# Performance work log

Hardware: AMD Instinct MI355X
Metric: run time of the kernel (lower is better)

## Reference

```python
import jax, jax.numpy as jnp
import numpy as np

D_MODEL = 512
HEAD_NUM = 8
EPS = 1e-5


def setup_inputs() -> dict:
    key = jax.random.key(0)
    ks = jax.random.split(key, 7)
    B, S, D = 2, 4096, D_MODEL
    scale = 1.0 / np.sqrt(D)
    return {
        "x": jax.random.normal(ks[0], (B, S, D), dtype=jnp.float32),
        "Wq": jax.random.normal(ks[1], (D, D), dtype=jnp.float32) * scale,
        "bq": jnp.zeros((D,), dtype=jnp.float32),
        "Wk": jax.random.normal(ks[2], (D, D), dtype=jnp.float32) * scale,
        "bk": jnp.zeros((D,), dtype=jnp.float32),
        "Wv": jax.random.normal(ks[3], (D, D), dtype=jnp.float32) * scale,
        "bv": jnp.zeros((D,), dtype=jnp.float32),
        "gamma": jnp.ones((D,), dtype=jnp.float32),
        "beta": jnp.zeros((D,), dtype=jnp.float32),
    }


def reference(x, Wq, bq, Wk, bk, Wv, bv, gamma, beta):
    B, S, D = x.shape
    H = HEAD_NUM
    hd = D // H  # q_k_head_dim == v_head_dim == 64
    q = (x @ Wq + bq).reshape(B, H, S, hd)  # faithful to torch .view (no transpose)
    k = (x @ Wk + bk).reshape(B, H, S, hd)
    v = (x @ Wv + bv).reshape(B, H, S, hd)
    # [B,H,S,S] score matrix, materialized exactly as the original does
    scores = jnp.einsum("bhqd,bhkd->bhqk", q, k) / jnp.sqrt(jnp.float32(hd))
    attn_w = jax.nn.softmax(scores, axis=-1)
    attn = jnp.einsum("bhqk,bhkd->bhqd", attn_w, v).reshape(B, S, D)
    h = x + attn
    mu = jnp.mean(h, axis=-1, keepdims=True)
    var = jnp.var(h, axis=-1, keepdims=True)
    y = (h - mu) / jnp.sqrt(var + EPS) * gamma + beta
    return y
```

## Files before the change

### kernel.cpp

```cpp
#include <hip/hip_runtime.h>
#include <stdint.h>

#define D_ 512
#define S_ 4096
#define HD 64
#define CHUNK (S_*HD)

typedef short short8 __attribute__((ext_vector_type(8)));
typedef unsigned short ushort8 __attribute__((ext_vector_type(8)));
typedef float f32x16 __attribute__((ext_vector_type(16)));
typedef float f32x4 __attribute__((ext_vector_type(4)));

__device__ __forceinline__ float b2f(unsigned short u){
  unsigned x = ((unsigned)u) << 16;
  return __builtin_bit_cast(float, x);
}
__device__ __forceinline__ unsigned short f2b(float f){
  unsigned x = __builtin_bit_cast(unsigned, f);
  return (unsigned short)((x + 0x7fffu + ((x >> 16) & 1u)) >> 16);
}
__device__ __forceinline__ unsigned cvt_pk_bf16(float lo, float hi){
  unsigned r; asm("v_cvt_pk_bf16_f32 %0, %1, %2" : "=v"(r) : "v"(lo), "v"(hi)); return r;
}
__device__ __forceinline__ float fexp2(float x){
  float r; asm("v_exp_f32 %0, %1" : "=v"(r) : "v"(x)); return r;
}
__device__ __forceinline__ void gload16(const void* g, void* l){
  __builtin_amdgcn_global_load_lds((__attribute__((address_space(1))) void*)g,
                                   (__attribute__((address_space(3))) void*)l, 16, 0, 0);
}

__global__ void k_convert(const float* __restrict__ x, unsigned short* __restrict__ xb,
                          const float* __restrict__ Wq, const float* __restrict__ Wk,
                          const float* __restrict__ Wv, unsigned short* __restrict__ wt){
  __shared__ __align__(16) float t[32][33];
  if (blockIdx.x < 2048){
    int i = blockIdx.x * blockDim.x + threadIdx.x;
    const float4* xv = (const float4*)x;
    float4 a = xv[i*2], b = xv[i*2+1];
    ushort8 o;
    o[0]=f2b(a.x); o[1]=f2b(a.y); o[2]=f2b(a.z); o[3]=f2b(a.w);
    o[4]=f2b(b.x); o[5]=f2b(b.y); o[6]=f2b(b.z); o[7]=f2b(b.w);
    ((ushort8*)xb)[i] = o;
    return;
  }
  const int i = blockIdx.x - 2048;
  const int z = i >> 8, rem = i & 255;
  const int k0 = (rem & 15) * 32, n0 = (rem >> 4) * 32;
  const float* W = (z==0) ? Wq : ((z==1) ? Wk : Wv);
  unsigned short* o = wt + z * D_ * D_;
  int r = threadIdx.x >> 3, c4 = (threadIdx.x & 7) * 4;
  float4 vv = *(const float4*)&W[(k0+r)*D_ + n0 + c4];
  t[r][c4+0]=vv.x; t[r][c4+1]=vv.y; t[r][c4+2]=vv.z; t[r][c4+3]=vv.w;
  __syncthreads();
  unsigned short* dst = &o[(n0+r)*D_ + k0 + c4];
  dst[0]=f2b(t[c4+0][r]); dst[1]=f2b(t[c4+1][r]);
  dst[2]=f2b(t[c4+2][r]); dst[3]=f2b(t[c4+3][r]);
}

__global__ void __launch_bounds__(256) k_gemm(const unsigned short* __restrict__ xb,
                                              const unsigned short* __restrict__ wt,
                                              const float* __restrict__ bq,
                                              const float* __restrict__ bk,
                                              const float* __restrict__ bv,
                                              unsigned short* __restrict__ q,
                                              unsigned short* __restrict__ k,
                                              unsigned short* __restrict__ v){
  __shared__ __align__(16) unsigned short At[2][128*32];
  __shared__ __align__(16) unsigned short Bt[2][128*32];
  const int bid = blockIdx.x;
  const int swz = (bid & 7) * 96 + (bid >> 3);
  const int mat = swz >> 8;
  const int rem = swz & 255;
  const int bx = rem >> 2, by = rem & 3;
  const unsigned short* w = wt + mat * D_ * D_;
  const float* bias = (mat==0) ? bq : ((mat==1) ? bk : bv);
  unsigned short* out = (mat==0) ? q : ((mat==1) ? k : v);
  const int m0 = bx * 128, n0 = by * 128;
  const int tid = threadIdx.x, lane = tid & 63, wv = tid >> 6;
  const int wm = wv >> 1, wn = wv & 1;
  const int l15 = lane & 15, l4 = lane >> 4;

  f32x4 acc[4][4] = {};

  auto stage = [&](int kt, int sel){
    const int kbase = kt * 32;
    #pragma unroll
    for (int j = 0; j < 2; j++){
      const int loff = wv*2048 + j*1024 + lane*16;
      const int row = loff >> 6;
      const int c = (loff >> 4) & 3;
      gload16(xb + (m0+row)*D_ + kbase + ((c ^ (row&3)) << 3),
              (char*)At[sel] + wv*2048 + j*1024);
      gload16(w  + (n0+row)*D_ + kbase + ((c ^ (row&3)) << 3),
              (char*)Bt[sel] + wv*2048 + j*1024);
    }
  };

  stage(0, 0);
  int buf = 0;
  for (int kt = 0; kt < 16; ++kt){
    __syncthreads();
    if (kt + 1 < 16) stage(kt + 1, buf ^ 1);
    short8 af[4], bf[4];
    #pragma unroll
    for (int mf = 0; mf < 4; mf++){
      const int row = wm*64 + mf*16 + l15;
      af[mf] = *(const short8*)((const char*)At[buf] + row*64 + ((l4*16) ^ ((row&3)<<4)));
    }
    #pragma unroll
    for (int nf = 0; nf < 4; nf++){
      const int row = wn*64 + nf*16 + l15;
      bf[nf] = *(const short8*)((const char*)Bt[buf] + row*64 + ((l4*16) ^ ((row&3)<<4)));
    }
    #pragma unroll
    for (int mf = 0; mf < 4; mf++)
      #pragma unroll
      for (int nf = 0; nf < 4; nf++)
        acc[mf][nf] = __builtin_amdgcn_mfma_f32_16x16x32_bf16(af[mf], bf[nf], acc[mf][nf], 0,0,0);
    buf ^= 1;
  }
  #pragma unroll
  for (int nf = 0; nf < 4; nf++){
    const int n = n0 + wn*64 + nf*16 + l15;
    const float bval = bias[n];
    #pragma unroll
    for (int mf = 0; mf < 4; mf++){
      #pragma unroll
      for (int r = 0; r < 4; r++){
        const int m = m0 + wm*64 + mf*16 + l4*4 + r;
        out[m*D_ + n] = f2b(acc[mf][nf][r] + bval);
      }
    }
  }
}

__global__ void k_transpose_v(const unsigned short* __restrict__ v, unsigned short* __restrict__ vt){
  __shared__ __align__(16) unsigned short t[64][72];
  const int bh = blockIdx.y, s0 = blockIdx.x * 64;
  const unsigned short* vc = v + bh * CHUNK;
  unsigned short* vtc = vt + bh * CHUNK;
  const int tid = threadIdx.x;
  #pragma unroll
  for (int j = 0; j < 2; j++){
    const int e = j*2048 + tid*8;
    const int row = e >> 6, col = e & 63;
    *(ushort8*)&t[row][col] = *(const ushort8*)&vc[(s0+row)*HD + col];
  }
  __syncthreads();
  const int d = tid >> 2, sc0 = (tid & 3) * 16;
  ushort8 o0, o1;
  #pragma unroll
  for (int j = 0; j < 4; j++){
    o0[j]   = t[sc0 + j     ][d];
    o0[j+4] = t[sc0 + 8 + j ][d];
    o1[j]   = t[sc0 + 4 + j ][d];
    o1[j+4] = t[sc0 + 12 + j][d];
  }
  *(ushort8*)&vtc[d*S_ + s0 + sc0]     = o0;
  *(ushort8*)&vtc[d*S_ + s0 + sc0 + 8] = o1;
}

__global__ void __launch_bounds__(256, 4) k_attn_part(const unsigned short* __restrict__ q,
                                                      const unsigned short* __restrict__ k,
                                                      const unsigned short* __restrict__ vt,
                                                      unsigned short* __restrict__ Op0,
                                                      unsigned short* __restrict__ Op1,
                                                      float2* __restrict__ ml0,
                                                      float2* __restrict__ ml1){
  __shared__ __align__(16) char smem[32768];
  const int bid = blockIdx.x;
  const int c8 = bid & 7, j = bid >> 3;
  const int bh   = 2*c8 + (j & 1);
  const int qblk = (j >> 1) & 31;
  const int half = (j >> 6) & 1;

  const int tid = threadIdx.x, lane = tid & 63, wv = tid >> 6;
  const int l31 = lane & 31, hi = lane >> 5;
  const unsigned short* qc  = q  + bh * CHUNK;
  const unsigned short* kc  = k  + bh * CHUNK;
  const unsigned short* vtc = vt + bh * CHUNK;
  unsigned short* Op = half ? Op1 : Op0;
  float2* ml = half ? ml1 : ml0;
  const int q0 = qblk * 128 + wv * 32;
  const int kvbase = half * 2048;

  short8 qf[4];
  {
    const int row = q0 + l31;
    #pragma unroll
    for (int kb = 0; kb < 4; kb++){
      ushort8 raw = *(const ushort8*)(qc + row*HD + kb*16 + hi*8);
      union { ushort8 u; short8 s; } cc;
      #pragma unroll
      for (int jj = 0; jj < 8; jj++) cc.u[jj] = f2b(b2f(raw[jj]) * (0.125f * 1.44269504f));
      qf[kb] = cc.s;
    }
  }
  short8 ones;
  #pragma unroll
  for (int jj = 0; jj < 8; jj++) ones[jj] = (short)0x3F80;

  f32x16 o0 = {}; f32x16 o1 = {};
  f32x16 lacc = {};
  float mrun = -__builtin_inff();

  auto stage = [&](int t, int sel){
    const int kv0 = kvbase + t * 64;
    char* kb_ = smem + sel*8192 + wv*2048;
    char* vb_ = smem + 16384 + sel*8192 + wv*2048;
    #pragma unroll
    for (int jj = 0; jj < 2; jj++){
      const int loff = wv*2048 + jj*1024 + lane*16;
      const int row = loff >> 7;
      const int c = (loff >> 4) & 7;
      gload16(kc  + (kv0+row)*HD + ((c ^ (row&7)) << 3), kb_ + jj*1024);
      gload16(vtc + row*S_ + kv0 + ((c ^ (row&7)) << 3), vb_ + jj*1024);
    }
  };

  stage(0, 0);
  int buf = 0;
  const int NT = 2048 / 64;
  for (int t = 0; t < NT; ++t){
    __syncthreads();
    if (t + 1 < NT) stage(t + 1, buf ^ 1);
    const char* kbuf = smem + buf*8192;
    const char* vbuf = smem + 16384 + buf*8192;

    f32x16 st0 = {}; f32x16 st1 = {};
    const int xr = (l31 & 7) << 4;
    #pragma unroll
    for (int kb = 0; kb < 4; kb++){
      const int off = kb*32 + hi*16;
      short8 kf0 = *(const short8*)(kbuf + l31*128        + (off ^ xr));
      short8 kf1 = *(const short8*)(kbuf + (32+l31)*128   + (off ^ xr));
      st0 = __builtin_amdgcn_mfma_f32_32x32x16_bf16(kf0, qf[kb], st0, 0,0,0);
      st1 = __builtin_amdgcn_mfma_f32_32x32x16_bf16(kf1, qf[kb], st1, 0,0,0);
    }

    float n0_ = fmaxf(fmaxf(st0[0], st0[1]),  st0[2]);
    float n1_ = fmaxf(fmaxf(st0[3], st0[4]),  st0[5]);
    float n2_ = fmaxf(fmaxf(st0[6], st0[7]),  st0[8]);
    float n3_ = fmaxf(fmaxf(st0[9], st0[10]), st0[11]);
    float n4_ = fmaxf(fmaxf(st0[12],st0[13]), st0[14]);
    float n5_ = fmaxf(fmaxf(st0[15],st1[0]),  st1[1]);
    float n6_ = fmaxf(fmaxf(st1[2], st1[3]),  st1[4]);
    float n7_ = fmaxf(fmaxf(st1[5], st1[6]),  st1[7]);
    float n8_ = fmaxf(fmaxf(st1[8], st1[9]),  st1[10]);
    float n9_ = fmaxf(fmaxf(st1[11],st1[12]), st1[13]);
    float nA_ = fmaxf(st1[14], st1[15]);
    n0_ = fmaxf(fmaxf(n0_, n1_), n2_);
    n3_ = fmaxf(fmaxf(n3_, n4_), n5_);
    n6_ = fmaxf(fmaxf(n6_, n7_), n8_);
    n9_ = fmaxf(n9_, nA_);
    float pm = fmaxf(fmaxf(fmaxf(n0_, n3_), n6_), n9_);
    pm = fmaxf(pm, __shfl_xor(pm, 32));

    if (!__all(pm <= mrun + 10.0f)){
      const float mn = fmaxf(mrun, pm);
      const float corr = fexp2(mrun - mn);
      mrun = mn;
      lacc[0] *= corr;
      o0 *= corr; o1 *= corr;
    }

    st0 -= mrun;
    st1 -= mrun;
    #pragma unroll
    for (int r = 0; r < 16; r++){
      st0[r] = fexp2(st0[r]);
      st1[r] = fexp2(st1[r]);
    }

    short8 pf[4];
    #pragma unroll
    for (int kb = 0; kb < 4; kb++){
      const f32x16& s = (kb < 2) ? st0 : st1;
      const int rb = (kb & 1) * 8;
      union { unsigned u[4]; short8 s8; } pu;
      pu.u[0] = cvt_pk_bf16(s[rb+0], s[rb+1]);
      pu.u[1] = cvt_pk_bf16(s[rb+2], s[rb+3]);
      pu.u[2] = cvt_pk_bf16(s[rb+4], s[rb+5]);
      pu.u[3] = cvt_pk_bf16(s[rb+6], s[rb+7]);
      pf[kb] = pu.s8;
    }

    #pragma unroll
    for (int kb = 0; kb < 4; kb++){
      const int off = kb*32 + hi*16;
      short8 vf0 = *(const short8*)(vbuf + l31*128      + (off ^ xr));
      short8 vf1 = *(const short8*)(vbuf + (32+l31)*128 + (off ^ xr));
      o0   = __builtin_amdgcn_mfma_f32_32x32x16_bf16(vf0, pf[kb], o0, 0,0,0);
      o1   = __builtin_amdgcn_mfma_f32_32x32x16_bf16(vf1, pf[kb], o1, 0,0,0);
      lacc = __builtin_amdgcn_mfma_f32_32x32x16_bf16(ones, pf[kb], lacc, 0,0,0);
    }
    buf ^= 1;
  }

  __syncthreads();
  {
    float* po = (float*)(void*)smem + wv*2048;
    #pragma unroll
    for (int r = 0; r < 16; r++){
      const int d = (r&3) + 8*(r>>2) + 4*hi;
      po[l31*64 + d]      = o0[r];
      po[l31*64 + 32 + d] = o1[r];
    }
  }
  if (hi == 0){
    ml[bh*S_ + q0 + l31] = make_float2(mrun, lacc[0]);
  }
  __syncthreads();
  {
    const int rr = lane >> 1, hf = lane & 1;
    const float* prow = (const float*)(void*)smem + wv*2048 + rr*64 + hf*32;
    unsigned short* dst = Op + (bh*S_ + q0 + rr)*HD + hf*32;
    #pragma unroll
    for (int blk = 0; blk < 4; blk++){
      ushort8 w8;
      #pragma unroll
      for (int jj = 0; jj < 8; jj++) w8[jj] = f2b(prow[blk*8 + jj]);
      *(ushort8*)(dst + blk*8) = w8;
    }
  }
}

__global__ void k_merge_ln(const unsigned short* __restrict__ Op0,
                           const unsigned short* __restrict__ Op1,
                           const float2* __restrict__ ml0,
                           const float2* __restrict__ ml1,
                           const float* __restrict__ x,
                           const float* __restrict__ gamma,
                           const float* __restrict__ beta,
                           float* __restrict__ out){
  const int row = blockIdx.x * 4 + (threadIdx.x >> 6);
  const int lane = threadIdx.x & 63;
  const int bh = row >> 9;
  const int s_attn = ((row & 511) << 3) + (lane >> 3);
  const int d0 = (lane & 7) * 8;
  const int oidx = (bh*S_ + s_attn)*HD + d0;
  ushort8 u0 = *(const ushort8*)(Op0 + oidx);
  ushort8 u1 = *(const ushort8*)(Op1 + oidx);
  const float2 a = ml0[bh*S_ + s_attn];
  const float2 c = ml1[bh*S_ + s_attn];
  const float M  = fmaxf(a.x, c.x);
  const float e1 = exp2f(a.x - M), e2 = exp2f(c.x - M);
  const float inv = 1.0f / (e1*a.y + e2*c.y);
  const float w1 = e1 * inv, w2 = e2 * inv;

  const float* xr = x + row*D_ + lane*8;
  float4 a0 = *(const float4*)xr, a1 = *(const float4*)(xr + 4);
  float h[8];
  h[0]=a0.x; h[1]=a0.y; h[2]=a0.z; h[3]=a0.w; h[4]=a1.x; h[5]=a1.y; h[6]=a1.z; h[7]=a1.w;
  #pragma unroll
  for (int jj = 0; jj < 8; jj++) h[jj] += w1*b2f(u0[jj]) + w2*b2f(u1[jj]);

  float sm = 0.f, ss = 0.f;
  #pragma unroll
  for (int jj = 0; jj < 8; jj++){ sm += h[jj]; ss += h[jj]*h[jj]; }
  #pragma unroll
  for (int msk = 1; msk < 64; msk <<= 1){ sm += __shfl_xor(sm, msk); ss += __shfl_xor(ss, msk); }
  const float mu = sm * (1.f/512.f);
  const float var = ss * (1.f/512.f) - mu*mu;
  const float rs = rsqrtf(var + 1e-5f);
  const float* g = gamma + lane*8;
  const float* be = beta + lane*8;
  float4 w0, w3;
  w0.x = (h[0]-mu)*rs*g[0] + be[0];
  w0.y = (h[1]-mu)*rs*g[1] + be[1];
  w0.z = (h[2]-mu)*rs*g[2] + be[2];
  w0.w = (h[3]-mu)*rs*g[3] + be[3];
  w3.x = (h[4]-mu)*rs*g[4] + be[4];
  w3.y = (h[5]-mu)*rs*g[5] + be[5];
  w3.z = (h[6]-mu)*rs*g[6] + be[6];
  w3.w = (h[7]-mu)*rs*g[7] + be[7];
  float* op = out + row*D_ + lane*8;
  *(float4*)op = w0;
  *(float4*)(op + 4) = w3;
}

extern "C" void kernel_launch(void* const* d_in, const int* in_sizes, int n_in,
                              void* d_out, int out_size, void* d_ws, size_t ws_size,
                              hipStream_t stream){
  const float* x     = (const float*)d_in[0];
  const float* Wq    = (const float*)d_in[1];
  const float* bq    = (const float*)d_in[2];
  const float* Wk    = (const float*)d_in[3];
  const float* bk    = (const float*)d_in[4];
  const float* Wv    = (const float*)d_in[5];
  const float* bv    = (const float*)d_in[6];
  const float* gamma = (const float*)d_in[7];
  const float* beta  = (const float*)d_in[8];
  float* out = (float*)d_out;

  char* ws = (char*)d_ws;
  unsigned short* wt = (unsigned short*)(ws);
  unsigned short* q  = (unsigned short*)(ws + 1572864);
  unsigned short* k  = (unsigned short*)(ws + 9961472);
  unsigned short* v  = (unsigned short*)(ws + 18350080);
  unsigned short* vt = (unsigned short*)(ws + 26738688);
  unsigned short* Op0 = v;
  unsigned short* Op1 = (unsigned short*)(ws + 35127296);
  float2* ml0 = (float2*)(ws + 43515904);
  float2* ml1 = (float2*)(ws + 44040192);
  unsigned short* xb = (unsigned short*)((char*)d_out + 8388608);

  k_convert    <<<2816, 256, 0, stream>>>(x, xb, Wq, Wk, Wv, wt);
  k_gemm       <<<768, 256, 0, stream>>>(xb, wt, bq, bk, bv, q, k, v);
  k_transpose_v<<<dim3(64,16),   256, 0, stream>>>(v, vt);
  k_attn_part  <<<1024, 256, 0, stream>>>(q, k, vt, Op0, Op1, ml0, ml1);
  k_merge_ln   <<<2048, 256, 0, stream>>>(Op0, Op1, ml0, ml1, x, gamma, beta, out);
}
```

Before: 131.2 us.

## Split attention KV range three ways and compute row sums on VALU

The attention kernel now splits the key/value range into three uneven parts (22/21/21 tiles) instead of two, launching 1536 blocks rather than 1024 to fill the GPU better. It raises the launch-bounds occupancy hint from 4 to 5. The ones-matrix MFMA that accumulated the softmax denominator is replaced by a per-lane sum and a cross-half shuffle. The first partial is stored as fp32 in the output buffer, and the merge kernel combines three partials. This adds one more partial read and larger fp32 traffic for the first split, and it aliases the output buffer as scratch.

```diff
diff --git a/kernel.cpp b/kernel.cpp
--- a/kernel.cpp
+++ b/kernel.cpp
@@ -161,29 +161,31 @@
   *(ushort8*)&vtc[d*S_ + s0 + sc0 + 8] = o1;
 }
 
-__global__ void __launch_bounds__(256, 4) k_attn_part(const unsigned short* __restrict__ q,
+__global__ void __launch_bounds__(256, 5) k_attn_part(const unsigned short* __restrict__ q,
                                                       const unsigned short* __restrict__ k,
                                                       const unsigned short* __restrict__ vt,
-                                                      unsigned short* __restrict__ Op0,
+                                                      float* __restrict__ Op0,
                                                       unsigned short* __restrict__ Op1,
+                                                      unsigned short* __restrict__ Op2,
                                                       float2* __restrict__ ml0,
-                                                      float2* __restrict__ ml1){
+                                                      float2* __restrict__ ml1,
+                                                      float2* __restrict__ ml2){
   __shared__ __align__(16) char smem[32768];
   const int bid = blockIdx.x;
   const int c8 = bid & 7, j = bid >> 3;
-  const int bh   = 2*c8 + (j & 1);
-  const int qblk = (j >> 1) & 31;
-  const int half = (j >> 6) & 1;
+  const int bh    = 2*c8 + (j & 1);
+  const int qblk  = (j >> 1) & 31;
+  const int third = j >> 6;
 
   const int tid = threadIdx.x, lane = tid & 63, wv = tid >> 6;
   const int l31 = lane & 31, hi = lane >> 5;
   const unsigned short* qc  = q  + bh * CHUNK;
   const unsigned short* kc  = k  + bh * CHUNK;
   const unsigned short* vtc = vt + bh * CHUNK;
-  unsigned short* Op = half ? Op1 : Op0;
-  float2* ml = half ? ml1 : ml0;
   const int q0 = qblk * 128 + wv * 32;
-  const int kvbase = half * 2048;
+  const int NT = (third == 0) ? 22 : 21;
+  const int kvbase = (third == 0) ? 0 : (1408 + (third - 1) * 1344);
+  float2* ml = (third == 0) ? ml0 : ((third == 1) ? ml1 : ml2);
 
   short8 qf[4];
   {
@@ -197,13 +199,9 @@
       qf[kb] = cc.s;
     }
   }
-  short8 ones;
-  #pragma unroll
-  for (int jj = 0; jj < 8; jj++) ones[jj] = (short)0x3F80;
 
   f32x16 o0 = {}; f32x16 o1 = {};
-  f32x16 lacc = {};
-  float mrun = -__builtin_inff();
+  float mrun = -__builtin_inff(), lrun = 0.f;
 
   auto stage = [&](int t, int sel){
     const int kv0 = kvbase + t * 64;
@@ -221,7 +219,6 @@
 
   stage(0, 0);
   int buf = 0;
-  const int NT = 2048 / 64;
   for (int t = 0; t < NT; ++t){
     __syncthreads();
     if (t + 1 < NT) stage(t + 1, buf ^ 1);
@@ -261,17 +258,23 @@
       const float mn = fmaxf(mrun, pm);
       const float corr = fexp2(mrun - mn);
       mrun = mn;
-      lacc[0] *= corr;
+      lrun *= corr;
       o0 *= corr; o1 *= corr;
     }
 
     st0 -= mrun;
     st1 -= mrun;
-    #pragma unroll
-    for (int r = 0; r < 16; r++){
-      st0[r] = fexp2(st0[r]);
-      st1[r] = fexp2(st1[r]);
-    }
+    float s0a = 0.f, s1a = 0.f, s2a = 0.f, s3a = 0.f;
+    #pragma unroll
+    for (int r = 0; r < 8; r++){
+      st0[r]   = fexp2(st0[r]);   s0a += st0[r];
+      st0[r+8] = fexp2(st0[r+8]); s1a += st0[r+8];
+      st1[r]   = fexp2(st1[r]);   s2a += st1[r];
+      st1[r+8] = fexp2(st1[r+8]); s3a += st1[r+8];
+    }
+    float sum = (s0a + s1a) + (s2a + s3a);
+    sum += __shfl_xor(sum, 32);
+    lrun += sum;
 
     short8 pf[4];
     #pragma unroll
@@ -291,9 +294,8 @@
       const int off = kb*32 + hi*16;
       short8 vf0 = *(const short8*)(vbuf + l31*128      + (off ^ xr));
       short8 vf1 = *(const short8*)(vbuf + (32+l31)*128 + (off ^ xr));
-      o0   = __builtin_amdgcn_mfma_f32_32x32x16_bf16(vf0, pf[kb], o0, 0,0,0);
-      o1   = __builtin_amdgcn_mfma_f32_32x32x16_bf16(vf1, pf[kb], o1, 0,0,0);
-      lacc = __builtin_amdgcn_mfma_f32_32x32x16_bf16(ones, pf[kb], lacc, 0,0,0);
+      o0 = __builtin_amdgcn_mfma_f32_32x32x16_bf16(vf0, pf[kb], o0, 0,0,0);
+      o1 = __builtin_amdgcn_mfma_f32_32x32x16_bf16(vf1, pf[kb], o1, 0,0,0);
     }
     buf ^= 1;
   }
@@ -309,52 +311,68 @@
     }
   }
   if (hi == 0){
-    ml[bh*S_ + q0 + l31] = make_float2(mrun, lacc[0]);
+    ml[bh*S_ + q0 + l31] = make_float2(mrun, lrun);
   }
   __syncthreads();
   {
     const int rr = lane >> 1, hf = lane & 1;
     const float* prow = (const float*)(void*)smem + wv*2048 + rr*64 + hf*32;
-    unsigned short* dst = Op + (bh*S_ + q0 + rr)*HD + hf*32;
-    #pragma unroll
-    for (int blk = 0; blk < 4; blk++){
-      ushort8 w8;
+    if (third == 0){
+      float* dst = Op0 + (size_t)(bh*S_ + q0 + rr)*HD + hf*32;
       #pragma unroll
-      for (int jj = 0; jj < 8; jj++) w8[jj] = f2b(prow[blk*8 + jj]);
-      *(ushort8*)(dst + blk*8) = w8;
-    }
-  }
-}
-
-__global__ void k_merge_ln(const unsigned short* __restrict__ Op0,
+      for (int blk = 0; blk < 8; blk++)
+        *(float4*)(dst + blk*4) = *(const float4*)(prow + blk*4);
+    } else {
+      unsigned short* Opb = (third == 1) ? Op1 : Op2;
+      unsigned short* dst = Opb + (bh*S_ + q0 + rr)*HD + hf*32;
+      #pragma unroll
+      for (int blk = 0; blk < 4; blk++){
+        ushort8 w8;
+        #pragma unroll
+        for (int jj = 0; jj < 8; jj++) w8[jj] = f2b(prow[blk*8 + jj]);
+        *(ushort8*)(dst + blk*8) = w8;
+      }
+    }
+  }
+}
+
+__global__ void k_merge_ln(const float* Op0,
                            const unsigned short* __restrict__ Op1,
+                           const unsigned short* __restrict__ Op2,
                            const float2* __restrict__ ml0,
                            const float2* __restrict__ ml1,
+                           const float2* __restrict__ ml2,
                            const float* __restrict__ x,
                            const float* __restrict__ gamma,
                            const float* __restrict__ beta,
-                           float* __restrict__ out){
+                           float* out){
   const int row = blockIdx.x * 4 + (threadIdx.x >> 6);
   const int lane = threadIdx.x & 63;
   const int bh = row >> 9;
   const int s_attn = ((row & 511) << 3) + (lane >> 3);
   const int d0 = (lane & 7) * 8;
   const int oidx = (bh*S_ + s_attn)*HD + d0;
-  ushort8 u0 = *(const ushort8*)(Op0 + oidx);
+  float4 f0a = *(const float4*)(Op0 + oidx);
+  float4 f0b = *(const float4*)(Op0 + oidx + 4);
   ushort8 u1 = *(const ushort8*)(Op1 + oidx);
+  ushort8 u2 = *(const ushort8*)(Op2 + oidx);
   const float2 a = ml0[bh*S_ + s_attn];
-  const float2 c = ml1[bh*S_ + s_attn];
-  const float M  = fmaxf(a.x, c.x);
-  const float e1 = exp2f(a.x - M), e2 = exp2f(c.x - M);
-  const float inv = 1.0f / (e1*a.y + e2*c.y);
-  const float w1 = e1 * inv, w2 = e2 * inv;
+  const float2 b = ml1[bh*S_ + s_attn];
+  const float c = 0.f;
+  const float2 cc = ml2[bh*S_ + s_attn];
+  (void)c;
+  const float M  = fmaxf(fmaxf(a.x, b.x), cc.x);
+  const float e0 = exp2f(a.x - M), e1 = exp2f(b.x - M), e2 = exp2f(cc.x - M);
+  const float inv = 1.0f / (e0*a.y + e1*b.y + e2*cc.y);
+  const float w0_ = e0 * inv, w1_ = e1 * inv, w2_ = e2 * inv;
 
   const float* xr = x + row*D_ + lane*8;
   float4 a0 = *(const float4*)xr, a1 = *(const float4*)(xr + 4);
   float h[8];
-  h[0]=a0.x; h[1]=a0.y; h[2]=a0.z; h[3]=a0.w; h[4]=a1.x; h[5]=a1.y; h[6]=a1.z; h[7]=a1.w;
-  #pragma unroll
-  for (int jj = 0; jj < 8; jj++) h[jj] += w1*b2f(u0[jj]) + w2*b2f(u1[jj]);
+  h[0]=a0.x + w0_*f0a.x; h[1]=a0.y + w0_*f0a.y; h[2]=a0.z + w0_*f0a.z; h[3]=a0.w + w0_*f0a.w;
+  h[4]=a1.x + w0_*f0b.x; h[5]=a1.y + w0_*f0b.y; h[6]=a1.z + w0_*f0b.z; h[7]=a1.w + w0_*f0b.w;
+  #pragma unroll
+  for (int jj = 0; jj < 8; jj++) h[jj] += w1_*b2f(u1[jj]) + w2_*b2f(u2[jj]);
 
   float sm = 0.f, ss = 0.f;
   #pragma unroll
@@ -400,15 +418,17 @@
   unsigned short* k  = (unsigned short*)(ws + 9961472);
   unsigned short* v  = (unsigned short*)(ws + 18350080);
   unsigned short* vt = (unsigned short*)(ws + 26738688);
-  unsigned short* Op0 = v;
-  unsigned short* Op1 = (unsigned short*)(ws + 35127296);
+  unsigned short* Op1 = v;
+  unsigned short* Op2 = (unsigned short*)(ws + 35127296);
   float2* ml0 = (float2*)(ws + 43515904);
   float2* ml1 = (float2*)(ws + 44040192);
+  float2* ml2 = (float2*)(ws + 44564480);
+  float* Op0 = out;
   unsigned short* xb = (unsigned short*)((char*)d_out + 8388608);
 
   k_convert    <<<2816, 256, 0, stream>>>(x, xb, Wq, Wk, Wv, wt);
   k_gemm       <<<768, 256, 0, stream>>>(xb, wt, bq, bk, bv, q, k, v);
   k_transpose_v<<<dim3(64,16),   256, 0, stream>>>(v, vt);
-  k_attn_part  <<<1024, 256, 0, stream>>>(q, k, vt, Op0, Op1, ml0, ml1);
-  k_merge_ln   <<<2048, 256, 0, stream>>>(Op0, Op1, ml0, ml1, x, gamma, beta, out);
-}
+  k_attn_part  <<<1536, 256, 0, stream>>>(q, k, vt, Op0, Op1, Op2, ml0, ml1, ml2);
+  k_merge_ln   <<<2048, 256, 0, stream>>>(Op0, Op1, Op2, ml0, ml1, ml2, x, gamma, beta, out);
+}
```

After: 181.1 us. 38.0% more time.
